# Kernel optimization log

Measured on AMD Instinct MI355X. Metric: run time of the kernel, lower is better.

Reference implementation:

```python
import jax, jax.numpy as jnp
import numpy as np

D_MODEL = 2048
N_HEAD = 16
N_KV_HEAD = 4
D_HEAD = D_MODEL // N_HEAD          # 128
N_REP = N_HEAD // N_KV_HEAD        # 4
B, S = 2, 2048


def setup_inputs() -> dict:
    key = jax.random.key(0)
    ks = jax.random.split(key, 7)
    x = jax.random.normal(ks[0], (B, S, D_MODEL), dtype=jnp.float32)
    cos = jax.random.uniform(ks[1], (S, D_HEAD // 2), dtype=jnp.float32)
    sin = jax.random.uniform(ks[2], (S, D_HEAD // 2), dtype=jnp.float32)
    sc = 1.0 / np.sqrt(D_MODEL)
    # weights stored as [in, out] so projection is x @ W
    wq = jax.random.normal(ks[3], (D_MODEL, D_MODEL), dtype=jnp.float32) * sc
    wk = jax.random.normal(ks[4], (D_MODEL, N_KV_HEAD * D_HEAD), dtype=jnp.float32) * sc
    wv = jax.random.normal(ks[5], (D_MODEL, N_KV_HEAD * D_HEAD), dtype=jnp.float32) * sc
    wo = jax.random.normal(ks[6], (D_MODEL, D_MODEL), dtype=jnp.float32) * sc
    return {"x": x, "cos": cos, "sin": sin, "wq": wq, "wk": wk, "wv": wv, "wo": wo}


def _apply_rope(t, cos, sin):
    # t: [B, H, S, D_HEAD]; cos/sin: [S, D_HEAD//2]
    d = t.shape[-1] // 2
    t1, t2 = t[..., :d], t[..., d:]
    c = cos[None, None, :, :]
    s = sin[None, None, :, :]
    return jnp.concatenate([t1 * c - t2 * s, t2 * c + t1 * s], axis=-1)


def reference(x, cos, sin, wq, wk, wv, wo):
    b, s, _ = x.shape
    q = (x @ wq).reshape(b, s, N_HEAD, D_HEAD).transpose(0, 2, 1, 3)      # [B,H,S,d]
    k = (x @ wk).reshape(b, s, N_KV_HEAD, D_HEAD).transpose(0, 2, 1, 3)   # [B,Hk,S,d]
    v = (x @ wv).reshape(b, s, N_KV_HEAD, D_HEAD).transpose(0, 2, 1, 3)
    q = _apply_rope(q, cos, sin)
    k = _apply_rope(k, cos, sin)
    # group query heads by shared kv head (repeat_interleave => consecutive groups)
    qg = q.reshape(b, N_KV_HEAD, N_REP, s, D_HEAD)
    scale = 1.0 / jnp.sqrt(jnp.asarray(D_HEAD, dtype=q.dtype))
    scores = jnp.einsum('bkrsd,bktd->bkrst', qg, k) * scale               # [B,Hk,r,S,S]
    causal = jnp.tril(jnp.ones((s, s), dtype=bool))
    scores = jnp.where(causal, scores, jnp.asarray(-jnp.inf, dtype=scores.dtype))
    attn = jax.nn.softmax(scores, axis=-1)
    out = jnp.einsum('bkrst,bktd->bkrsd', attn, v)                        # [B,Hk,r,S,d]
    out = out.reshape(b, N_HEAD, s, D_HEAD).transpose(0, 2, 1, 3).reshape(b, s, D_MODEL)
    return out @ wo
```

## Files before the change

kernel.cpp:

```cpp
#include <hip/hip_runtime.h>
#include <stdint.h>

#define D_MODEL 2048
#define NHEAD 16
#define NKV 4
#define DHEAD 128
#define BB 2
#define SS 2048
#define MROWS (BB*SS)
#define NQKV 3072

typedef __bf16 bf16x8_t __attribute__((ext_vector_type(8)));
typedef float f32x4_t __attribute__((ext_vector_type(4)));
typedef float f32x16_t __attribute__((ext_vector_type(16)));
typedef unsigned short u16x8_t __attribute__((ext_vector_type(8)));
typedef unsigned short u16x4_t __attribute__((ext_vector_type(4)));
typedef unsigned int u32x4_t __attribute__((ext_vector_type(4)));

__device__ __forceinline__ unsigned short f2bf(float f) {
    return __builtin_bit_cast(unsigned short, (__bf16)f);
}
__device__ __forceinline__ float bf2f(unsigned short h) {
    union { uint32_t u; float f; } v; v.u = ((uint32_t)h) << 16;
    return v.f;
}
__device__ __forceinline__ unsigned int pack_bf2(float lo, float hi) {
    return (unsigned int)f2bf(lo) | ((unsigned int)f2bf(hi) << 16);
}

__device__ __forceinline__ void stage16(const unsigned short* g, unsigned short* l) {
    auto gp = (const __attribute__((address_space(1))) unsigned short*)(uintptr_t)g;
    auto lp = (__attribute__((address_space(3))) unsigned short*)(uint32_t)(uintptr_t)l;
    __builtin_amdgcn_global_load_lds(gp, lp, 16, 0, 0);
}
__device__ __forceinline__ bf16x8_t lds_frag(const unsigned short* p) {
    return __builtin_bit_cast(bf16x8_t, *(const u16x8_t*)p);
}

#define BAR()   do { __builtin_amdgcn_s_barrier(); asm volatile("" ::: "memory"); } while (0)
#define WAITL() asm volatile("s_waitcnt lgkmcnt(0)" ::: "memory")

__global__ void k_convert(const float* __restrict__ in, unsigned short* __restrict__ out, int n4) {
    int stride = gridDim.x * blockDim.x;
    for (int idx = blockIdx.x * blockDim.x + threadIdx.x; idx < n4; idx += stride) {
        float4 f = ((const float4*)in)[idx];
        u16x4_t o;
        o[0] = f2bf(f.x); o[1] = f2bf(f.y); o[2] = f2bf(f.z); o[3] = f2bf(f.w);
        ((u16x4_t*)out)[idx] = o;
    }
}

__global__ __launch_bounds__(256) void k_transpose(const float* __restrict__ in,
                                                   unsigned short* __restrict__ out,
                                                   int R, int C) {
    __shared__ unsigned short tile[64][72];
    const int c0 = blockIdx.x * 64, r0 = blockIdx.y * 64;
    const int t = threadIdx.x;
    #pragma unroll
    for (int i = 0; i < 4; i++) {
        int g = i * 256 + t;
        int r = g >> 4, c4 = (g & 15) * 4;
        float4 f = *(const float4*)&in[(size_t)(r0 + r) * C + c0 + c4];
        tile[r][c4 + 0] = f2bf(f.x); tile[r][c4 + 1] = f2bf(f.y);
        tile[r][c4 + 2] = f2bf(f.z); tile[r][c4 + 3] = f2bf(f.w);
    }
    __syncthreads();
    #pragma unroll
    for (int i = 0; i < 2; i++) {
        int g = i * 256 + t;
        int oc = g >> 3, r8 = (g & 7) * 8;
        u16x8_t o;
        #pragma unroll
        for (int k = 0; k < 8; k++) o[k] = tile[r8 + k][oc];
        *(u16x8_t*)&out[(size_t)(c0 + oc) * R + r0 + r8] = o;
    }
}

__global__ void k_rope(const unsigned short* __restrict__ in, const float* __restrict__ cosb,
                       const float* __restrict__ sinb, unsigned short* __restrict__ out,
                       int nheads, int in_row_stride, float scale) {
    int idx = blockIdx.x * blockDim.x + threadIdx.x;
    int total = BB * SS * nheads * 64;
    if (idx >= total) return;
    int d  = idx & 63;
    int hh = (idx >> 6) % nheads;
    int bs = (idx >> 6) / nheads;
    int s  = bs % SS, b = bs / SS;
    const unsigned short* ip = in + (size_t)(b * SS + s) * in_row_stride + hh * 128 + d;
    float t1 = bf2f(ip[0]), t2 = bf2f(ip[64]);
    float c = cosb[s * 64 + d], sn = sinb[s * 64 + d];
    unsigned short* op = out + ((size_t)(b * nheads + hh) * SS + s) * 128 + d;
    op[0]  = f2bf((t1 * c - t2 * sn) * scale);
    op[64] = f2bf((t2 * c + t1 * sn) * scale);
}

__global__ __launch_bounds__(256) void k_vtrans(const unsigned short* __restrict__ src,
                                                unsigned short* __restrict__ vt,
                                                int stride, int colbase) {
    const int s0 = blockIdx.x * 64;
    const int kvb = blockIdx.y;
    const int b = kvb >> 2, kv = kvb & 3;
    __shared__ unsigned short tile[64][136];
    const int t = threadIdx.x;
    #pragma unroll
    for (int i = 0; i < 4; i++) {
        int g = i * 256 + t;
        int sr = g >> 4, c8 = (g & 15) * 8;
        u16x8_t v = *(const u16x8_t*)&src[(size_t)(b * SS + s0 + sr) * stride + colbase + kv * 128 + c8];
        #pragma unroll
        for (int k = 0; k < 8; k++) tile[sr][c8 + k] = v[k];
    }
    __syncthreads();
    unsigned short* obase = vt + (size_t)kvb * DHEAD * SS;
    #pragma unroll
    for (int i = 0; i < 4; i++) {
        int g = i * 256 + t;
        int d = g >> 3, s8 = (g & 7) * 8;
        u16x8_t o;
        #pragma unroll
        for (int k = 0; k < 8; k++) o[k] = tile[s8 + k][d];
        *(u16x8_t*)&obase[(size_t)d * SS + s0 + s8] = o;
    }
}

template <bool OUTF32>
__global__ __launch_bounds__(512, 2) void k_gemm8(const unsigned short* __restrict__ A,
                                                  const unsigned short* __restrict__ Bt,
                                                  void* __restrict__ Cout,
                                                  int N, int K, int ntn) {
    __shared__ __align__(16) unsigned short As[2][256 * 64];
    __shared__ __align__(16) unsigned short Bs[2][256 * 64];
    const int nwg = gridDim.x, wg = blockIdx.x;
    const int qq = nwg >> 3, rr = nwg & 7;
    const int xcd = wg & 7, sid = wg >> 3;
    const int swg = (xcd < rr ? xcd * (qq + 1) : rr * (qq + 1) + (xcd - rr) * qq) + sid;
    const int m0 = (swg / ntn) * 256, n0 = (swg % ntn) * 256;

    const int tid = threadIdx.x, lane = tid & 63, wid = tid >> 6;
    const int lr = lane & 15, lg = lane >> 4;
    const int wr = (wid >> 2) * 128, wc = (wid & 3) * 64;
    const int NT = K >> 6;

    auto stage = [&](int tile, int pos) {
        int srcTile = tile < NT ? tile : NT - 1;
        bool isA = (pos == 0) || (pos == 3);
        int half = (pos >= 2) ? 1 : 0;
        const unsigned short* base = isA ? A : Bt;
        int row0 = (isA ? m0 : n0) + half * 128;
        unsigned short* lbase = (isA ? As[tile & 1] : Bs[tile & 1]) + half * 8192;
        int k0 = srcTile * 64;
        #pragma unroll
        for (int i = 0; i < 2; i++) {
            int g = i * 512 + tid;
            int row = g >> 3, p = g & 7;
            stage16(&base[(size_t)(row0 + row) * K + k0 + ((p ^ (row & 7)) * 8)],
                    &lbase[(i * 512 + wid * 64) * 8]);
        }
    };

    bf16x8_t aA[4][2], bLo[2][2], bHi[2][2];
    f32x4_t acc[8][4] = {};

    stage(0, 0); stage(0, 3); stage(0, 1); stage(0, 2);
    stage(1, 1); stage(1, 2);
    asm volatile("s_waitcnt vmcnt(4)" ::: "memory");
    BAR();

    for (int t = 0; t < NT; t++) {
        const unsigned short* as = As[t & 1];
        const unsigned short* bs = Bs[t & 1];
        #pragma unroll
        for (int i = 0; i < 4; i++)
          #pragma unroll
          for (int kk = 0; kk < 2; kk++) {
            int R = wr + i * 16 + lr;
            aA[i][kk] = lds_frag(&as[R * 64 + (((kk * 4 + lg) ^ (R & 7)) * 8)]);
          }
        #pragma unroll
        for (int j = 0; j < 2; j++)
          #pragma unroll
          for (int kk = 0; kk < 2; kk++) {
            int R = wc + j * 16 + lr;
            bLo[j][kk] = lds_frag(&bs[R * 64 + (((kk * 4 + lg) ^ (R & 7)) * 8)]);
          }
        stage(t + 1, 0);
        BAR(); WAITL();
        __builtin_amdgcn_s_setprio(1);
        #pragma unroll
        for (int kk = 0; kk < 2; kk++)
          #pragma unroll
          for (int i = 0; i < 4; i++)
            #pragma unroll
            for (int j = 0; j < 2; j++)
              acc[i][j] = __builtin_amdgcn_mfma_f32_16x16x32_bf16(aA[i][kk], bLo[j][kk], acc[i][j], 0, 0, 0);
        __builtin_amdgcn_s_setprio(0);
        BAR();
        #pragma unroll
        for (int j = 0; j < 2; j++)
          #pragma unroll
          for (int kk = 0; kk < 2; kk++) {
            int R = wc + (2 + j) * 16 + lr;
            bHi[j][kk] = lds_frag(&bs[R * 64 + (((kk * 4 + lg) ^ (R & 7)) * 8)]);
          }
        stage(t + 1, 3);
        BAR(); WAITL();
        __builtin_amdgcn_s_setprio(1);
        #pragma unroll
        for (int kk = 0; kk < 2; kk++)
          #pragma unroll
          for (int i = 0; i < 4; i++)
            #pragma unroll
            for (int j = 0; j < 2; j++)
              acc[i][2 + j] = __builtin_amdgcn_mfma_f32_16x16x32_bf16(aA[i][kk], bHi[j][kk], acc[i][2 + j], 0, 0, 0);
        __builtin_amdgcn_s_setprio(0);
        BAR();
        #pragma unroll
        for (int i = 0; i < 4; i++)
          #pragma unroll
          for (int kk = 0; kk < 2; kk++) {
            int R = wr + (4 + i) * 16 + lr;
            aA[i][kk] = lds_frag(&as[R * 64 + (((kk * 4 + lg) ^ (R & 7)) * 8)]);
          }
        stage(t + 2, 1);
        BAR(); WAITL();
        __builtin_amdgcn_s_setprio(1);
        #pragma unroll
        for (int kk = 0; kk < 2; kk++)
          #pragma unroll
          for (int i = 0; i < 4; i++)
            #pragma unroll
            for (int j = 0; j < 2; j++)
              acc[4 + i][2 + j] = __builtin_amdgcn_mfma_f32_16x16x32_bf16(aA[i][kk], bHi[j][kk], acc[4 + i][2 + j], 0, 0, 0);
        __builtin_amdgcn_s_setprio(0);
        BAR();
        stage(t + 2, 2);
        asm volatile("s_waitcnt vmcnt(4)" ::: "memory");
        BAR(); WAITL();
        __builtin_amdgcn_s_setprio(1);
        #pragma unroll
        for (int kk = 0; kk < 2; kk++)
          #pragma unroll
          for (int i = 0; i < 4; i++)
            #pragma unroll
            for (int j = 0; j < 2; j++)
              acc[4 + i][j] = __builtin_amdgcn_mfma_f32_16x16x32_bf16(aA[i][kk], bLo[j][kk], acc[4 + i][j], 0, 0, 0);
        __builtin_amdgcn_s_setprio(0);
        BAR();
    }

    #pragma unroll
    for (int m = 0; m < 8; m++)
      #pragma unroll
      for (int n = 0; n < 4; n++)
        #pragma unroll
        for (int r = 0; r < 4; r++) {
            int row = m0 + wr + m * 16 + lg * 4 + r;
            int col = n0 + wc + n * 16 + lr;
            if constexpr (OUTF32) ((float*)Cout)[(size_t)row * N + col] = acc[m][n][r];
            else ((unsigned short*)Cout)[(size_t)row * N + col] = f2bf(acc[m][n][r]);
        }
}

__global__ __launch_bounds__(256, 2) void k_attn(const unsigned short* __restrict__ qb,
                                                 const unsigned short* __restrict__ kb,
                                                 const unsigned short* __restrict__ vt,
                                                 unsigned short* __restrict__ ab) {
    const int bid = blockIdx.x;
    const int u = bid & 255;
    const int t = (bid < 256) ? (u >> 5) : (15 - (u >> 5));
    const int h = u & 15, b = (u >> 4) & 1;
    const int kvh = h >> 2;
    const int tid = threadIdx.x, lane = tid & 63, wid = tid >> 6;
    const int ql = lane & 31, hi = lane >> 5;
    const int swzq = ql & 7;
    __shared__ __align__(16) unsigned short k_lds[2][64 * 128];
    __shared__ __align__(16) unsigned short v_lds[2][128 * 64];
    __shared__ float sm_lds[128];

    const unsigned short* qbase = qb + (size_t)(b * NHEAD + h) * SS * DHEAD;
    const unsigned short* kbase = kb + (size_t)(b * NKV + kvh) * SS * DHEAD;
    const unsigned short* vbase = vt + (size_t)(b * NKV + kvh) * DHEAD * SS;

    auto stage_kv = [&](int j, int buf) {
        #pragma unroll
        for (int i = 0; i < 4; i++) {
            int g = i * 256 + wid * 64 + lane;
            int row = g >> 4, p = g & 15;
            stage16(&kbase[(size_t)(j * 64 + row) * DHEAD + ((p ^ (row & 7)) * 8)],
                    &k_lds[buf][(i * 256 + wid * 64) * 8]);
        }
        #pragma unroll
        for (int i = 0; i < 4; i++) {
            int g = i * 256 + wid * 64 + lane;
            int row = g >> 3, p = g & 7;
            stage16(&vbase[(size_t)row * SS + j * 64 + ((p ^ (row & 7)) * 8)],
                    &v_lds[buf][(i * 256 + wid * 64) * 8]);
        }
    };

    auto make_frag = [&](const f32x16_t& p, int base) -> bf16x8_t {
        unsigned int c01 = pack_bf2(p[base + 0], p[base + 1]);
        unsigned int c23 = pack_bf2(p[base + 2], p[base + 3]);
        unsigned int c45 = pack_bf2(p[base + 4], p[base + 5]);
        unsigned int c67 = pack_bf2(p[base + 6], p[base + 7]);
        unsigned int r1 = __shfl_xor(hi ? c01 : c45, 32);
        unsigned int r2 = __shfl_xor(hi ? c23 : c67, 32);
        u32x4_t w;
        w[0] = hi ? r1 : c01;
        w[1] = hi ? r2 : c23;
        w[2] = hi ? c45 : r1;
        w[3] = hi ? c67 : r2;
        return __builtin_bit_cast(bf16x8_t, w);
    };

    const int q0w = t * 128 + wid * 32;
    const int jend = 2 * t + 1;

    bf16x8_t qf[8];
    #pragma unroll
    for (int kk = 0; kk < 8; kk++)
        qf[kk] = __builtin_bit_cast(bf16x8_t,
            *(const u16x8_t*)&qbase[(size_t)(q0w + ql) * DHEAD + kk * 16 + hi * 8]);

    f32x16_t acc[4] = {};
    float m_i = -1e30f, l_i = 0.f;

    stage_kv(0, 0);
    asm volatile("s_waitcnt vmcnt(0)" ::: "memory");
    __syncthreads();

    #pragma unroll 1
    for (int j = 0; j <= jend; j++) {
        const int buf = j & 1;
        if (j < jend) stage_kv(j + 1, buf ^ 1);
        if ((q0w + 31) >= (j << 6)) {
            const unsigned short* kl = k_lds[buf];
            const unsigned short* vl = v_lds[buf];
            f32x16_t p0 = {}, p1 = {};
            #pragma unroll
            for (int kk = 0; kk < 8; kk++) {
                int c = ((2 * kk + hi) ^ swzq) * 8;
                bf16x8_t k0 = lds_frag(&kl[ql * 128 + c]);
                bf16x8_t k1 = lds_frag(&kl[(32 + ql) * 128 + c]);
                p0 = __builtin_amdgcn_mfma_f32_32x32x16_bf16(k0, qf[kk], p0, 0, 0, 0);
                p1 = __builtin_amdgcn_mfma_f32_32x32x16_bf16(k1, qf[kk], p1, 0, 0, 0);
            }
            if ((j << 6) + 63 > q0w) {
                const int qg = q0w + ql;
                const int kvb = (j << 6) + 4 * hi;
                #pragma unroll
                for (int r = 0; r < 16; r++) {
                    int kvg = kvb + (r & 3) + 8 * (r >> 2);
                    if (kvg > qg) p0[r] = -1e30f;
                    if (kvg + 32 > qg) p1[r] = -1e30f;
                }
            }
            float mx = p0[0];
            #pragma unroll
            for (int r = 1; r < 16; r++) mx = fmaxf(mx, p0[r]);
            #pragma unroll
            for (int r = 0; r < 16; r++) mx = fmaxf(mx, p1[r]);
            mx = fmaxf(mx, __shfl_xor(mx, 32));
            if (__any(mx - m_i > 8.0f)) {
                float mnew = fmaxf(m_i, mx);
                float alpha = exp2f(m_i - mnew);
                l_i *= alpha; m_i = mnew;
                if (lane < 32) sm_lds[wid * 32 + lane] = alpha;
                WAITL();
                #pragma unroll
                for (int r = 0; r < 16; r++) {
                    float ar = sm_lds[wid * 32 + (r & 3) + 8 * (r >> 2) + 4 * hi];
                    #pragma unroll
                    for (int d = 0; d < 4; d++) acc[d][r] *= ar;
                }
            }
            float sum = 0.f;
            #pragma unroll
            for (int r = 0; r < 16; r++) { float v = exp2f(p0[r] - m_i); p0[r] = v; sum += v; }
            #pragma unroll
            for (int r = 0; r < 16; r++) { float v = exp2f(p1[r] - m_i); p1[r] = v; sum += v; }
            sum += __shfl_xor(sum, 32);
            l_i += sum;
            bf16x8_t pa[4];
            pa[0] = make_frag(p0, 0);
            pa[1] = make_frag(p0, 8);
            pa[2] = make_frag(p1, 0);
            pa[3] = make_frag(p1, 8);
            #pragma unroll
            for (int ks = 0; ks < 4; ks++) {
                int cv = ((2 * ks + hi) ^ swzq) * 8;
                #pragma unroll
                for (int d = 0; d < 4; d++) {
                    bf16x8_t bv = lds_frag(&vl[(d * 32 + ql) * 64 + cv]);
                    acc[d] = __builtin_amdgcn_mfma_f32_32x32x16_bf16(pa[ks], bv, acc[d], 0, 0, 0);
                }
            }
        }
        asm volatile("s_waitcnt vmcnt(0)" ::: "memory");
        __syncthreads();
    }

    if (lane < 32) sm_lds[wid * 32 + lane] = l_i;
    WAITL();
    #pragma unroll
    for (int r = 0; r < 16; r++) {
        float li = sm_lds[wid * 32 + (r & 3) + 8 * (r >> 2) + 4 * hi];
        float rl = 1.0f / li;
        int rowg = q0w + (r & 3) + 8 * (r >> 2) + 4 * hi;
        #pragma unroll
        for (int d = 0; d < 4; d++)
            ab[((size_t)b * SS + rowg) * D_MODEL + h * DHEAD + d * 32 + ql] =
                f2bf(acc[d][r] * rl);
    }
}

extern "C" void kernel_launch(void* const* d_in, const int* in_sizes, int n_in,
                              void* d_out, int out_size, void* d_ws, size_t ws_size,
                              hipStream_t stream) {
    const float* x    = (const float*)d_in[0];
    const float* cosb = (const float*)d_in[1];
    const float* sinb = (const float*)d_in[2];
    const float* wq   = (const float*)d_in[3];
    const float* wk   = (const float*)d_in[4];
    const float* wv   = (const float*)d_in[5];
    const float* wo   = (const float*)d_in[6];

    char* ws = (char*)d_ws;
    unsigned short* xb    = (unsigned short*)(ws + (size_t)0);
    unsigned short* wqkvT = (unsigned short*)(ws + ((size_t)16 << 20));
    unsigned short* woT   = (unsigned short*)(ws + ((size_t)28 << 20));
    unsigned short* qkvg  = (unsigned short*)(ws + ((size_t)36 << 20));
    unsigned short* qbuf  = (unsigned short*)(ws + ((size_t)60 << 20));
    unsigned short* kbuf  = (unsigned short*)(ws + ((size_t)76 << 20));
    unsigned short* vtb   = (unsigned short*)(ws + ((size_t)80 << 20));
    unsigned short* abuf  = qkvg;

    k_convert<<<2048, 256, 0, stream>>>(x, xb, MROWS * D_MODEL / 4);
    k_transpose<<<dim3(32, 32), 256, 0, stream>>>(wq, wqkvT, D_MODEL, D_MODEL);
    k_transpose<<<dim3(8, 32), 256, 0, stream>>>(wk, wqkvT + (size_t)2048 * D_MODEL, D_MODEL, 512);
    k_transpose<<<dim3(8, 32), 256, 0, stream>>>(wv, wqkvT + (size_t)2560 * D_MODEL, D_MODEL, 512);
    k_transpose<<<dim3(32, 32), 256, 0, stream>>>(wo, woT, D_MODEL, D_MODEL);

    k_gemm8<false><<<16 * 12, 512, 0, stream>>>(xb, wqkvT, qkvg, NQKV, D_MODEL, 12);

    k_rope<<<(BB * SS * NHEAD * 64) / 256, 256, 0, stream>>>(qkvg, cosb, sinb, qbuf, NHEAD, NQKV,
                                                             0.12751743f);
    k_rope<<<(BB * SS * NKV * 64) / 256, 256, 0, stream>>>(qkvg + 2048, cosb, sinb, kbuf, NKV, NQKV, 1.0f);
    k_vtrans<<<dim3(32, 8), 256, 0, stream>>>(qkvg, vtb, NQKV, 2560);

    k_attn<<<512, 256, 0, stream>>>(qbuf, kbuf, vtb, abuf);

    k_gemm8<true><<<16 * 8, 512, 0, stream>>>(abuf, woT, (float*)d_out, D_MODEL, D_MODEL, 8);
}
```

Baseline: 226.8 us.

## Fuse Q RoPE into attention, add half-tile output GEMM, raise MFMA priority

Removes the separate RoPE kernel for Q and instead applies rotary embedding and the softmax scale while loading Q fragments inside the attention kernel. The attention output buffer moves to its own workspace region. A new GEMM variant with 128x256 tiles launches twice as many workgroups for the output projection, which gives the machine more parallelism for that small-N GEMM. MFMA loops in attention are wrapped with s_setprio. The cost is extra per-block Q loads of cos/sin and a more complex GEMM schedule.

```diff
diff --git a/kernel.cpp b/kernel.cpp
--- a/kernel.cpp
+++ b/kernel.cpp
@@ -261,7 +261,145 @@
         }
 }
 
-__global__ __launch_bounds__(256, 2) void k_attn(const unsigned short* __restrict__ qb,
+template <bool OUTF32>
+__global__ __launch_bounds__(512, 2) void k_gemm8h(const unsigned short* __restrict__ A,
+                                                   const unsigned short* __restrict__ Bt,
+                                                   void* __restrict__ Cout,
+                                                   int N, int K, int ntn) {
+    __shared__ __align__(16) unsigned short As[2][128 * 64];
+    __shared__ __align__(16) unsigned short Bs[2][256 * 64];
+    const int nwg = gridDim.x, wg = blockIdx.x;
+    const int qq = nwg >> 3, rr = nwg & 7;
+    const int xcd = wg & 7, sid = wg >> 3;
+    const int swg = (xcd < rr ? xcd * (qq + 1) : rr * (qq + 1) + (xcd - rr) * qq) + sid;
+    const int m0 = (swg / ntn) * 128, n0 = (swg % ntn) * 256;
+
+    const int tid = threadIdx.x, lane = tid & 63, wid = tid >> 6;
+    const int lr = lane & 15, lg = lane >> 4;
+    const int wr = (wid >> 2) * 64, wc = (wid & 3) * 64;
+    const int NT = K >> 6;
+
+    auto stage = [&](int tile, int pos) {
+        int srcTile = tile < NT ? tile : NT - 1;
+        bool isA = (pos == 0);
+        const unsigned short* base = isA ? A : Bt;
+        int row0 = isA ? m0 : (n0 + (pos - 1) * 128);
+        unsigned short* lbase = isA ? As[tile & 1] : (Bs[tile & 1] + (pos - 1) * 8192);
+        int k0 = srcTile * 64;
+        #pragma unroll
+        for (int i = 0; i < 2; i++) {
+            int g = i * 512 + tid;
+            int row = g >> 3, p = g & 7;
+            stage16(&base[(size_t)(row0 + row) * K + k0 + ((p ^ (row & 7)) * 8)],
+                    &lbase[(i * 512 + wid * 64) * 8]);
+        }
+    };
+
+    bf16x8_t aA[2][2], bLo[2][2], bHi[2][2];
+    f32x4_t acc[4][4] = {};
+
+    stage(0, 0); stage(0, 1); stage(0, 2);
+    stage(1, 1); stage(1, 2);
+    asm volatile("s_waitcnt vmcnt(4)" ::: "memory");
+    BAR();
+
+    for (int t = 0; t < NT; t++) {
+        const unsigned short* as = As[t & 1];
+        const unsigned short* bs = Bs[t & 1];
+        #pragma unroll
+        for (int i = 0; i < 2; i++)
+          #pragma unroll
+          for (int kk = 0; kk < 2; kk++) {
+            int R = wr + i * 16 + lr;
+            aA[i][kk] = lds_frag(&as[R * 64 + (((kk * 4 + lg) ^ (R & 7)) * 8)]);
+          }
+        #pragma unroll
+        for (int j = 0; j < 2; j++)
+          #pragma unroll
+          for (int kk = 0; kk < 2; kk++) {
+            int R = wc + j * 16 + lr;
+            bLo[j][kk] = lds_frag(&bs[R * 64 + (((kk * 4 + lg) ^ (R & 7)) * 8)]);
+          }
+        stage(t + 1, 0);
+        BAR(); WAITL();
+        __builtin_amdgcn_s_setprio(1);
+        #pragma unroll
+        for (int kk = 0; kk < 2; kk++)
+          #pragma unroll
+          for (int i = 0; i < 2; i++)
+            #pragma unroll
+            for (int j = 0; j < 2; j++)
+              acc[i][j] = __builtin_amdgcn_mfma_f32_16x16x32_bf16(aA[i][kk], bLo[j][kk], acc[i][j], 0, 0, 0);
+        __builtin_amdgcn_s_setprio(0);
+        BAR();
+        #pragma unroll
+        for (int j = 0; j < 2; j++)
+          #pragma unroll
+          for (int kk = 0; kk < 2; kk++) {
+            int R = wc + (2 + j) * 16 + lr;
+            bHi[j][kk] = lds_frag(&bs[R * 64 + (((kk * 4 + lg) ^ (R & 7)) * 8)]);
+          }
+        BAR(); WAITL();
+        __builtin_amdgcn_s_setprio(1);
+        #pragma unroll
+        for (int kk = 0; kk < 2; kk++)
+          #pragma unroll
+          for (int i = 0; i < 2; i++)
+            #pragma unroll
+            for (int j = 0; j < 2; j++)
+              acc[i][2 + j] = __builtin_amdgcn_mfma_f32_16x16x32_bf16(aA[i][kk], bHi[j][kk], acc[i][2 + j], 0, 0, 0);
+        __builtin_amdgcn_s_setprio(0);
+        BAR();
+        #pragma unroll
+        for (int i = 0; i < 2; i++)
+          #pragma unroll
+          for (int kk = 0; kk < 2; kk++) {
+            int R = wr + (2 + i) * 16 + lr;
+            aA[i][kk] = lds_frag(&as[R * 64 + (((kk * 4 + lg) ^ (R & 7)) * 8)]);
+          }
+        stage(t + 2, 1);
+        BAR(); WAITL();
+        __builtin_amdgcn_s_setprio(1);
+        #pragma unroll
+        for (int kk = 0; kk < 2; kk++)
+          #pragma unroll
+          for (int i = 0; i < 2; i++)
+            #pragma unroll
+            for (int j = 0; j < 2; j++)
+              acc[2 + i][2 + j] = __builtin_amdgcn_mfma_f32_16x16x32_bf16(aA[i][kk], bHi[j][kk], acc[2 + i][2 + j], 0, 0, 0);
+        __builtin_amdgcn_s_setprio(0);
+        BAR();
+        stage(t + 2, 2);
+        asm volatile("s_waitcnt vmcnt(4)" ::: "memory");
+        BAR(); WAITL();
+        __builtin_amdgcn_s_setprio(1);
+        #pragma unroll
+        for (int kk = 0; kk < 2; kk++)
+          #pragma unroll
+          for (int i = 0; i < 2; i++)
+            #pragma unroll
+            for (int j = 0; j < 2; j++)
+              acc[2 + i][j] = __builtin_amdgcn_mfma_f32_16x16x32_bf16(aA[i][kk], bLo[j][kk], acc[2 + i][j], 0, 0, 0);
+        __builtin_amdgcn_s_setprio(0);
+        BAR();
+    }
+
+    #pragma unroll
+    for (int m = 0; m < 4; m++)
+      #pragma unroll
+      for (int n = 0; n < 4; n++)
+        #pragma unroll
+        for (int r = 0; r < 4; r++) {
+            int row = m0 + wr + m * 16 + lg * 4 + r;
+            int col = n0 + wc + n * 16 + lr;
+            if constexpr (OUTF32) ((float*)Cout)[(size_t)row * N + col] = acc[m][n][r];
+            else ((unsigned short*)Cout)[(size_t)row * N + col] = f2bf(acc[m][n][r]);
+        }
+}
+
+__global__ __launch_bounds__(256, 2) void k_attn(const unsigned short* __restrict__ qg,
+                                                 const float* __restrict__ cosb,
+                                                 const float* __restrict__ sinb,
                                                  const unsigned short* __restrict__ kb,
                                                  const unsigned short* __restrict__ vt,
                                                  unsigned short* __restrict__ ab) {
@@ -277,7 +415,6 @@
     __shared__ __align__(16) unsigned short v_lds[2][128 * 64];
     __shared__ float sm_lds[128];
 
-    const unsigned short* qbase = qb + (size_t)(b * NHEAD + h) * SS * DHEAD;
     const unsigned short* kbase = kb + (size_t)(b * NKV + kvh) * SS * DHEAD;
     const unsigned short* vbase = vt + (size_t)(b * NKV + kvh) * DHEAD * SS;
 
@@ -314,13 +451,32 @@
     };
 
     const int q0w = t * 128 + wid * 32;
+    const int s_row = q0w + ql;
     const int jend = 2 * t + 1;
 
     bf16x8_t qf[8];
-    #pragma unroll
-    for (int kk = 0; kk < 8; kk++)
-        qf[kk] = __builtin_bit_cast(bf16x8_t,
-            *(const u16x8_t*)&qbase[(size_t)(q0w + ql) * DHEAD + kk * 16 + hi * 8]);
+    {
+        const unsigned short* qsrc = qg + (size_t)(b * SS + s_row) * NQKV + h * DHEAD;
+        const float SCALE = 0.12751743f;
+        #pragma unroll
+        for (int kk = 0; kk < 4; kk++) {
+            int dbase = kk * 16 + hi * 8;
+            u16x8_t r1 = *(const u16x8_t*)&qsrc[dbase];
+            u16x8_t r2 = *(const u16x8_t*)&qsrc[64 + dbase];
+            float4 c0 = *(const float4*)&cosb[(size_t)s_row * 64 + dbase];
+            float4 c1 = *(const float4*)&cosb[(size_t)s_row * 64 + dbase + 4];
+            float4 s0 = *(const float4*)&sinb[(size_t)s_row * 64 + dbase];
+            float4 s1 = *(const float4*)&sinb[(size_t)s_row * 64 + dbase + 4];
+            float cc[8] = {c0.x, c0.y, c0.z, c0.w, c1.x, c1.y, c1.z, c1.w};
+            float ss[8] = {s0.x, s0.y, s0.z, s0.w, s1.x, s1.y, s1.z, s1.w};
+            #pragma unroll
+            for (int e = 0; e < 8; e++) {
+                float t1 = bf2f(r1[e]), t2 = bf2f(r2[e]);
+                qf[kk][e]     = (__bf16)((t1 * cc[e] - t2 * ss[e]) * SCALE);
+                qf[kk + 4][e] = (__bf16)((t2 * cc[e] + t1 * ss[e]) * SCALE);
+            }
+        }
+    }
 
     f32x16_t acc[4] = {};
     float m_i = -1e30f, l_i = 0.f;
@@ -337,6 +493,7 @@
             const unsigned short* kl = k_lds[buf];
             const unsigned short* vl = v_lds[buf];
             f32x16_t p0 = {}, p1 = {};
+            __builtin_amdgcn_s_setprio(1);
             #pragma unroll
             for (int kk = 0; kk < 8; kk++) {
                 int c = ((2 * kk + hi) ^ swzq) * 8;
@@ -345,14 +502,15 @@
                 p0 = __builtin_amdgcn_mfma_f32_32x32x16_bf16(k0, qf[kk], p0, 0, 0, 0);
                 p1 = __builtin_amdgcn_mfma_f32_32x32x16_bf16(k1, qf[kk], p1, 0, 0, 0);
             }
+            __builtin_amdgcn_s_setprio(0);
             if ((j << 6) + 63 > q0w) {
-                const int qg = q0w + ql;
+                const int qg2 = q0w + ql;
                 const int kvb = (j << 6) + 4 * hi;
                 #pragma unroll
                 for (int r = 0; r < 16; r++) {
                     int kvg = kvb + (r & 3) + 8 * (r >> 2);
-                    if (kvg > qg) p0[r] = -1e30f;
-                    if (kvg + 32 > qg) p1[r] = -1e30f;
+                    if (kvg > qg2) p0[r] = -1e30f;
+                    if (kvg + 32 > qg2) p1[r] = -1e30f;
                 }
             }
             float mx = p0[0];
@@ -386,6 +544,7 @@
             pa[1] = make_frag(p0, 8);
             pa[2] = make_frag(p1, 0);
             pa[3] = make_frag(p1, 8);
+            __builtin_amdgcn_s_setprio(1);
             #pragma unroll
             for (int ks = 0; ks < 4; ks++) {
                 int cv = ((2 * ks + hi) ^ swzq) * 8;
@@ -395,6 +554,7 @@
                     acc[d] = __builtin_amdgcn_mfma_f32_32x32x16_bf16(pa[ks], bv, acc[d], 0, 0, 0);
                 }
             }
+            __builtin_amdgcn_s_setprio(0);
         }
         asm volatile("s_waitcnt vmcnt(0)" ::: "memory");
         __syncthreads();
@@ -430,10 +590,9 @@
     unsigned short* wqkvT = (unsigned short*)(ws + ((size_t)16 << 20));
     unsigned short* woT   = (unsigned short*)(ws + ((size_t)28 << 20));
     unsigned short* qkvg  = (unsigned short*)(ws + ((size_t)36 << 20));
-    unsigned short* qbuf  = (unsigned short*)(ws + ((size_t)60 << 20));
+    unsigned short* abuf  = (unsigned short*)(ws + ((size_t)60 << 20));
     unsigned short* kbuf  = (unsigned short*)(ws + ((size_t)76 << 20));
     unsigned short* vtb   = (unsigned short*)(ws + ((size_t)80 << 20));
-    unsigned short* abuf  = qkvg;
 
     k_convert<<<2048, 256, 0, stream>>>(x, xb, MROWS * D_MODEL / 4);
     k_transpose<<<dim3(32, 32), 256, 0, stream>>>(wq, wqkvT, D_MODEL, D_MODEL);
@@ -443,12 +602,10 @@
 
     k_gemm8<false><<<16 * 12, 512, 0, stream>>>(xb, wqkvT, qkvg, NQKV, D_MODEL, 12);
 
-    k_rope<<<(BB * SS * NHEAD * 64) / 256, 256, 0, stream>>>(qkvg, cosb, sinb, qbuf, NHEAD, NQKV,
-                                                             0.12751743f);
     k_rope<<<(BB * SS * NKV * 64) / 256, 256, 0, stream>>>(qkvg + 2048, cosb, sinb, kbuf, NKV, NQKV, 1.0f);
     k_vtrans<<<dim3(32, 8), 256, 0, stream>>>(qkvg, vtb, NQKV, 2560);
 
-    k_attn<<<512, 256, 0, stream>>>(qbuf, kbuf, vtb, abuf);
-
-    k_gemm8<true><<<16 * 8, 512, 0, stream>>>(abuf, woT, (float*)d_out, D_MODEL, D_MODEL, 8);
-}
+    k_attn<<<512, 256, 0, stream>>>(qkvg, cosb, sinb, kbuf, vtb, abuf);
+
+    k_gemm8h<true><<<32 * 8, 512, 0, stream>>>(abuf, woT, (float*)d_out, D_MODEL, D_MODEL, 8);
+}
```

Result: faster. 203.6 us, median of 4 (-10.2%).
